# Kernel tuning notes

Hardware: AMD Instinct MI355X
Metric: run time of the kernel (lower is better)

## Reference

```python
import jax, jax.numpy as jnp
import numpy as np

V, H, L, S, B = 32000, 1024, 4, 256, 16


def setup_inputs() -> dict:
    key = jax.random.key(0)
    ks = jax.random.split(key, 6)
    s = 0.02  # init scale
    return {
        "x": jax.random.randint(ks[0], (S, B), 0, V, dtype=jnp.int32),
        "h0": jnp.zeros((L, B, H), jnp.float32),
        "c0": jnp.zeros((L, B, H), jnp.float32),
        "emb": jax.random.normal(ks[1], (V, H), jnp.float32) * s,
        "W_ih": jax.random.normal(ks[2], (L, 4 * H, H), jnp.float32) * s,
        "W_hh": jax.random.normal(ks[3], (L, 4 * H, H), jnp.float32) * s,
        "b_ih": jnp.zeros((L, 4 * H), jnp.float32),
        "b_hh": jnp.zeros((L, 4 * H), jnp.float32),
        "fc_W": jax.random.normal(ks[4], (V, H), jnp.float32) * s,
        "fc_b": jnp.zeros((V,), jnp.float32),
    }


def _lstm_layer(xs, h0, c0, Wih, Whh, b):
    # xs: [S, B, Hin]; torch gate order is (i, f, g, o)
    def step(carry, x_t):
        h, c = carry
        z = x_t @ Wih.T + h @ Whh.T + b  # [B, 4H]
        i, f, g, o = jnp.split(z, 4, axis=-1)
        c = jax.nn.sigmoid(f) * c + jax.nn.sigmoid(i) * jnp.tanh(g)
        h = jax.nn.sigmoid(o) * jnp.tanh(c)
        return (h, c), h

    (hT, cT), ys = jax.lax.scan(step, (h0, c0), xs)
    return ys, hT, cT


def reference(x, h0, c0, emb, W_ih, W_hh, b_ih, b_hh, fc_W, fc_b):
    y = emb[x]  # [S, B, H]
    h_fin, c_fin = [], []
    for l in range(L):  # fixed small layer count; time dim handled by scan
        y, hT, cT = _lstm_layer(y, h0[l], c0[l], W_ih[l], W_hh[l], b_ih[l] + b_hh[l])
        h_fin.append(hT)
        c_fin.append(cT)
    logits = y @ fc_W.T + fc_b  # [S, B, V]
    return logits, jnp.stack(h_fin), jnp.stack(c_fin)
```

## Files before the change

kernel.cpp:

```cpp
#include <hip/hip_runtime.h>
#include <hip/hip_bf16.h>

typedef unsigned short u16;
typedef short short8 __attribute__((ext_vector_type(8)));
typedef u16 u16x8 __attribute__((ext_vector_type(8)));
typedef float f32x4 __attribute__((ext_vector_type(4)));

#define H 1024
#define NB 16
#define SEQ 256
#define NL 4
#define VOCAB 32000
#define G4 4096
#define YSZ ((size_t)SEQ * NB * H)

__device__ __forceinline__ u16 f2bf(float f) {
  __hip_bfloat16 h = __float2bfloat16(f);
  return *reinterpret_cast<u16*>(&h);
}
__device__ __forceinline__ float sigm(float x) { return 1.0f / (1.0f + __expf(-x)); }
__device__ __forceinline__ float tanhfast(float x) { return 2.0f / (1.0f + __expf(-2.0f * x)) - 1.0f; }

__device__ __forceinline__ f32x4 mfma16(short8 a, short8 b, f32x4 c) {
  return __builtin_amdgcn_mfma_f32_16x16x32_bf16(a, b, c, 0, 0, 0);
}

template <int BOFF>
__device__ __forceinline__ short8 ldg_sc(const u16* p) {
  short8 r;
  asm volatile("global_load_dwordx4 %0, %1, off offset:%2 sc0 sc1"
               : "=&v"(r) : "v"(p), "n"(BOFF));
  return r;
}
template <int BOFF>
__device__ __forceinline__ short8 ldg_ca(const u16* p) {
  short8 r;
  asm volatile("global_load_dwordx4 %0, %1, off offset:%2"
               : "=&v"(r) : "v"(p), "n"(BOFF));
  return r;
}

#define LD8SC(d, p)                                            \
  do {                                                         \
    d[0] = ldg_sc<0 * 64>(p); d[1] = ldg_sc<1 * 64>(p);        \
    d[2] = ldg_sc<2 * 64>(p); d[3] = ldg_sc<3 * 64>(p);        \
    d[4] = ldg_sc<4 * 64>(p); d[5] = ldg_sc<5 * 64>(p);        \
    d[6] = ldg_sc<6 * 64>(p); d[7] = ldg_sc<7 * 64>(p);        \
  } while (0)
#define LD8CA(d, p)                                            \
  do {                                                         \
    d[0] = ldg_ca<0 * 64>(p); d[1] = ldg_ca<1 * 64>(p);        \
    d[2] = ldg_ca<2 * 64>(p); d[3] = ldg_ca<3 * 64>(p);        \
    d[4] = ldg_ca<4 * 64>(p); d[5] = ldg_ca<5 * 64>(p);        \
    d[6] = ldg_ca<6 * 64>(p); d[7] = ldg_ca<7 * 64>(p);        \
  } while (0)


__global__ void cvt_bf16(const float* __restrict__ in, u16* __restrict__ out, int n8) {
  const int i = blockIdx.x * blockDim.x + threadIdx.x;
  if (i >= n8) return;
  const float4 a = ((const float4*)in)[2 * i];
  const float4 b = ((const float4*)in)[2 * i + 1];
  u16x8 o;
  o[0] = f2bf(a.x); o[1] = f2bf(a.y); o[2] = f2bf(a.z); o[3] = f2bf(a.w);
  o[4] = f2bf(b.x); o[5] = f2bf(b.y); o[6] = f2bf(b.z); o[7] = f2bf(b.w);
  *(u16x8*)(out + (size_t)i * 8) = o;
}

__global__ void bias_sum(const float* __restrict__ a, const float* __restrict__ b,
                         float* __restrict__ o, int n) {
  const int i = blockIdx.x * blockDim.x + threadIdx.x;
  if (i < n) o[i] = a[i] + b[i];
}

__global__ void zero_u32(unsigned* __restrict__ p, int n) {
  const int i = blockIdx.x * blockDim.x + threadIdx.x;
  if (i < n) p[i] = 0u;
}

__global__ void gather_emb(const int* __restrict__ x, const float* __restrict__ emb,
                           u16* __restrict__ Y) {
  const int row = blockIdx.x;
  const int tok = x[row];
  const float4 v = ((const float4*)(emb + (size_t)tok * H))[threadIdx.x];
  ushort4 o;
  o.x = f2bf(v.x); o.y = f2bf(v.y); o.z = f2bf(v.z); o.w = f2bf(v.w);
  *(ushort4*)(Y + (size_t)row * H + threadIdx.x * 4) = o;
}

__device__ __forceinline__ void pollboth_sp(const unsigned* __restrict__ xp, unsigned xt,
                                            const unsigned* __restrict__ hp, unsigned ht) {
  unsigned xv, hv;
  do {
    asm volatile("global_load_dword %0, %2, off sc0 sc1\n\t"
                 "global_load_dword %1, %3, off sc0 sc1\n\t"
                 "s_waitcnt vmcnt(0)"
                 : "=&v"(xv), "=&v"(hv) : "v"(xp), "v"(hp) : "memory");
  } while (!__all(xv >= xt && hv >= ht));
  __builtin_amdgcn_sched_barrier(0);
}


__global__ __launch_bounds__(256, 1) void lstm_scan(
    const u16* __restrict__ ybase_r, u16* __restrict__ ybase_w,
    const u16* __restrict__ Wih_all, const u16* __restrict__ Whh_all,
    const float* __restrict__ bias_all, const u16* __restrict__ h0_all,
    const float* __restrict__ c0_all, float* __restrict__ hfin_all,
    float* __restrict__ cfin_all, unsigned* __restrict__ bars)
{
  extern __shared__ u16 sm[];
  u16* __restrict__ smw = sm;
  f32x4* __restrict__ lred = (f32x4*)(sm + 65536);
  u16* __restrict__ smh = sm + 73728;

  const int tid = threadIdx.x;
  const int lane = tid & 63;
  const int wid = tid >> 6;
  const int l = blockIdx.x >> 6;
  const int jgrp = blockIdx.x & 63;
  const int jbase = jgrp * 16;
  const int b = lane & 15;
  const int lg = lane >> 4;
  const int m = lane & 15;
  const int j = jbase + wid * 4 + lg;

  const u16* __restrict__ Yin  = ybase_r + (size_t)l * YSZ;
  u16* __restrict__ Yout       = ybase_w + (size_t)(l + 1) * YSZ;
  const u16* __restrict__ Wih  = Wih_all + (size_t)l * G4 * H;
  const u16* __restrict__ Whh  = Whh_all + (size_t)l * G4 * H;
  const float* __restrict__ bias = bias_all + (size_t)l * G4;
  const u16* __restrict__ h0b  = h0_all + (size_t)l * NB * H;
  const float* __restrict__ c0 = c0_all + (size_t)l * NB * H;
  float* __restrict__ hfin     = hfin_all + (size_t)l * NB * H;
  float* __restrict__ cfin     = cfin_all + (size_t)l * NB * H;
  unsigned* __restrict__ myflags = bars + l * 1024;
  const unsigned* __restrict__ xflags = bars + (l > 0 ? (l - 1) : 0) * 1024;
  unsigned* __restrict__ myflag_wr = myflags + jgrp * 16;
  const unsigned* __restrict__ xfp = xflags + lane * 16;
  const unsigned* __restrict__ hfp = myflags + lane * 16;

  #pragma unroll
  for (int rt = 0; rt < 4; ++rt) {
    const size_t ar = (size_t)((m & 3) * H + jbase + rt * 4 + (m >> 2));
    const u16* src = Whh + ar * H + lg * 8;
    #pragma unroll
    for (int i = 0; i < 8; ++i) {
      const int ks = wid * 8 + i;
      short8 w = *(const short8*)(src + ks * 32);
      *(short8*)(smw + (size_t)rt * 16384 + (size_t)ks * 512 + lane * 8) = w;
    }
  }
  short8 WI[32];
  #pragma unroll
  for (int rt = 0; rt < 4; ++rt) {
    const size_t ar = (size_t)((m & 3) * H + jbase + rt * 4 + (m >> 2));
    const u16* src = Wih + ar * H + lg * 8;
    #pragma unroll
    for (int i = 0; i < 8; ++i) {
      WI[rt * 8 + i] = *(const short8*)(src + (wid * 8 + i) * 32);
      asm volatile("" : "+v"(WI[rt * 8 + i]));
    }
  }
  __syncthreads();

  f32x4 bias4;
  bias4[0] = bias[0 * H + j];
  bias4[1] = bias[1 * H + j];
  bias4[2] = bias[2 * H + j];
  bias4[3] = bias[3 * H + j];

  float c = c0[b * H + j];
  const int boff = b * H + lg * 8;
  const int kboff = wid * 256;
  const u16* __restrict__ smwv = smw + (size_t)wid * 4096 + lane * 8;

  for (int t = 0; t < SEQ; ++t) {
    const u16* xw = Yin + (size_t)t * (NB * H) + boff + kboff;
    const u16* hw = (t == 0 ? h0b : Yout + (size_t)(t - 1) * (NB * H)) + boff + kboff;

    const unsigned xt = (l > 0) ? (unsigned)(t + 1) : 0u;
    const unsigned ht = (unsigned)t;
    if ((xt | ht) != 0u) pollboth_sp(xfp, xt, hfp, ht);

    short8 fx[8], fh[8];
    if (l > 0) { LD8SC(fx, xw); } else { LD8CA(fx, xw); }
    if (t > 0) { LD8SC(fh, hw); } else { LD8CA(fh, hw); }

    asm volatile("s_waitcnt vmcnt(8)" ::: "memory");
    __builtin_amdgcn_sched_barrier(0);

    f32x4 a0 = {0.f, 0.f, 0.f, 0.f};
    f32x4 a1 = {0.f, 0.f, 0.f, 0.f};
    f32x4 a2 = {0.f, 0.f, 0.f, 0.f};
    f32x4 a3 = {0.f, 0.f, 0.f, 0.f};

    #pragma unroll
    for (int i = 0; i < 8; ++i) {
      a0 = mfma16(WI[0 * 8 + i], fx[i], a0);
      a1 = mfma16(WI[1 * 8 + i], fx[i], a1);
      a2 = mfma16(WI[2 * 8 + i], fx[i], a2);
      a3 = mfma16(WI[3 * 8 + i], fx[i], a3);
    }

    __builtin_amdgcn_sched_barrier(0);
    asm volatile("s_waitcnt vmcnt(0)" ::: "memory");
    __builtin_amdgcn_sched_barrier(0);

    #pragma unroll
    for (int i = 0; i < 8; ++i) {
      short8 w0 = *(const short8*)(smwv + 0 * 16384 + i * 512);
      short8 w1 = *(const short8*)(smwv + 1 * 16384 + i * 512);
      short8 w2 = *(const short8*)(smwv + 2 * 16384 + i * 512);
      short8 w3 = *(const short8*)(smwv + 3 * 16384 + i * 512);
      a0 = mfma16(w0, fh[i], a0);
      a1 = mfma16(w1, fh[i], a1);
      a2 = mfma16(w2, fh[i], a2);
      a3 = mfma16(w3, fh[i], a3);
    }

    if (wid != 0) lred[(0 * 4 + wid) * 64 + lane] = a0;
    if (wid != 1) lred[(1 * 4 + wid) * 64 + lane] = a1;
    if (wid != 2) lred[(2 * 4 + wid) * 64 + lane] = a2;
    if (wid != 3) lred[(3 * 4 + wid) * 64 + lane] = a3;
    __syncthreads();

    f32x4 z4 = bias4;
    if (wid == 0)      z4 += a0;
    else if (wid == 1) z4 += a1;
    else if (wid == 2) z4 += a2;
    else               z4 += a3;
    #pragma unroll
    for (int w2 = 0; w2 < 4; ++w2)
      if (w2 != wid) z4 += lred[(wid * 4 + w2) * 64 + lane];

    const float ig = sigm(z4[0]);
    const float fg = sigm(z4[1]);
    const float gg = tanhfast(z4[2]);
    const float og = sigm(z4[3]);
    c = fg * c + ig * gg;
    const float h = og * tanhfast(c);

    smh[b * 16 + wid * 4 + lg] = f2bf(h);
    if (t == SEQ - 1) {
      hfin[b * H + j] = h;
      cfin[b * H + j] = c;
    }

    __syncthreads();
    if (wid == 0) {
      if (lane < 32) {
        const int br = lane >> 1, half = lane & 1;
        u16x8 pv = *(const u16x8*)&smh[br * 16 + half * 8];
        const u16* dst = Yout + (size_t)t * (NB * H) + (size_t)br * H + jbase + half * 8;
        asm volatile("global_store_dwordx4 %0, %1, off sc0 sc1"
                     :: "v"(dst), "v"(pv) : "memory");
      }
      asm volatile("s_waitcnt vmcnt(0)" ::: "memory");
      if (lane == 0) {
        const unsigned tv = (unsigned)(t + 1);
        asm volatile("global_store_dword %0, %1, off sc0 sc1"
                     :: "v"(myflag_wr), "v"(tv) : "memory");
      }
    }
  }
}


__global__ __launch_bounds__(256, 1) void gemm_bt_bias(
    const u16* __restrict__ A, const u16* __restrict__ Bw,
    const float* __restrict__ bias, float* __restrict__ C, int N)
{
  __shared__ u16 As[128 * 64];
  __shared__ u16 Bs[128 * 64];
  const int tid = threadIdx.x;
  const int lane = tid & 63;
  const int wid = tid >> 6;
  const unsigned id = blockIdx.x + gridDim.x * blockIdx.y;
  const unsigned xcd = id & 7u, seq = id >> 3;
  const int m0 = (int)(xcd * 4 + (seq & 3u)) * 128;
  const int n0 = (int)(seq >> 2) * 128;
  const int wr = wid >> 1, wc = wid & 1;
  const int lr = lane >> 3;
  const int lc = (lane & 7) * 8;
  f32x4 acc[4][4] = {};

  for (int k0 = 0; k0 < H; k0 += 64) {
    __syncthreads();
    #pragma unroll
    for (int cc = 0; cc < 4; ++cc) {
      const int row = wid * 32 + cc * 8 + lr;
      __builtin_amdgcn_global_load_lds(
          (const __attribute__((address_space(1))) void*)(A + (size_t)(m0 + row) * H + k0 + lc),
          (__attribute__((address_space(3))) void*)(As + row * 64 + lc), 16, 0, 0);
      __builtin_amdgcn_global_load_lds(
          (const __attribute__((address_space(1))) void*)(Bw + (size_t)(n0 + row) * H + k0 + lc),
          (__attribute__((address_space(3))) void*)(Bs + row * 64 + lc), 16, 0, 0);
    }
    __syncthreads();
    #pragma unroll
    for (int ks = 0; ks < 2; ++ks) {
      short8 af[4], bfr[4];
      #pragma unroll
      for (int i = 0; i < 4; ++i) {
        af[i]  = *(const short8*)&As[(wr * 64 + i * 16 + (lane & 15)) * 64 + ks * 32 + (lane >> 4) * 8];
        bfr[i] = *(const short8*)&Bs[(wc * 64 + i * 16 + (lane & 15)) * 64 + ks * 32 + (lane >> 4) * 8];
      }
      #pragma unroll
      for (int i = 0; i < 4; ++i) {
        #pragma unroll
        for (int jj = 0; jj < 4; ++jj)
          acc[i][jj] = mfma16(af[i], bfr[jj], acc[i][jj]);
      }
    }
  }

  #pragma unroll
  for (int jj = 0; jj < 4; ++jj) {
    const int col = n0 + wc * 64 + jj * 16 + (lane & 15);
    const float bv = bias[col];
    #pragma unroll
    for (int i = 0; i < 4; ++i) {
      const int rbase = m0 + wr * 64 + i * 16 + (lane >> 4) * 4;
      #pragma unroll
      for (int r = 0; r < 4; ++r)
        C[(size_t)(rbase + r) * N + col] = acc[i][jj][r] + bv;
    }
  }
}


extern "C" void kernel_launch(void* const* d_in, const int* in_sizes, int n_in,
                              void* d_out, int out_size, void* d_ws, size_t ws_size,
                              hipStream_t stream) {
  const int*   x    = (const int*)d_in[0];
  const float* h0   = (const float*)d_in[1];
  const float* c0   = (const float*)d_in[2];
  const float* emb  = (const float*)d_in[3];
  const float* W_ih = (const float*)d_in[4];
  const float* W_hh = (const float*)d_in[5];
  const float* b_ih = (const float*)d_in[6];
  const float* b_hh = (const float*)d_in[7];
  const float* fc_W = (const float*)d_in[8];
  const float* fc_b = (const float*)d_in[9];
  float* out = (float*)d_out;
  char* ws = (char*)d_ws;

  size_t off = 0;
  u16* WihB = (u16*)(ws + off); off += (size_t)NL * G4 * H * 2;
  u16* WhhB = (u16*)(ws + off); off += (size_t)NL * G4 * H * 2;
  u16* fcWB = (u16*)(ws + off); off += (size_t)VOCAB * H * 2;
  u16* h0B  = (u16*)(ws + off); off += (size_t)NL * NB * H * 2;
  float* biasB = (float*)(ws + off); off += (size_t)NL * G4 * 4;
  u16* ybufs = (u16*)(ws + off); off += (size_t)(NL + 1) * YSZ * 2;
  unsigned* bars = (unsigned*)(ws + off); off += 16384;
  if (ws_size < off) return;

  int n8;
  n8 = NL * G4 * H / 8;  cvt_bf16<<<(n8 + 255) / 256, 256, 0, stream>>>(W_ih, WihB, n8);
  n8 = NL * G4 * H / 8;  cvt_bf16<<<(n8 + 255) / 256, 256, 0, stream>>>(W_hh, WhhB, n8);
  n8 = VOCAB * H / 8;    cvt_bf16<<<(n8 + 255) / 256, 256, 0, stream>>>(fc_W, fcWB, n8);
  n8 = NL * NB * H / 8;  cvt_bf16<<<(n8 + 255) / 256, 256, 0, stream>>>(h0, h0B, n8);
  bias_sum<<<(NL * G4 + 255) / 256, 256, 0, stream>>>(b_ih, b_hh, biasB, NL * G4);
  zero_u32<<<16, 256, 0, stream>>>(bars, 4096);
  gather_emb<<<SEQ * NB, 256, 0, stream>>>(x, emb, ybufs);

  float* hfin = out + (size_t)SEQ * NB * VOCAB;
  float* cfin = hfin + (size_t)NL * NB * H;

  lstm_scan<<<NL * 64, 256, 147968, stream>>>(
      ybufs, ybufs, WihB, WhhB, biasB, h0B, c0, hfin, cfin, bars);

  gemm_bt_bias<<<dim3(32, 250), 256, 0, stream>>>(
      ybufs + (size_t)NL * YSZ, fcWB, fc_b, out, VOCAB);
}
```

Before: 1.955 ms.

## Replace flag-based cross-block sync with sentinel-filled data polling

Drops the separate per-block step flags. The output Y buffers for layers 1-4 are now pre-filled with an all-ones sentinel, and consumers spin-load the actual h/x data until no 32-bit word equals the sentinel. This removes the flag store, its vmcnt(0) drain on the producer side and the flag-then-data round trip on the consumer side, so each step avoids a dependent global access. The risks are the extra fill kernel over 4 layers of Y, heavier polling traffic because full data tiles are re-read on every retry, and correctness depending on bf16 pairs never naturally encoding as 0xFFFFFFFF (a NaN pattern) and on the 16-byte stores landing atomically.

```diff
diff --git a/kernel.cpp b/kernel.cpp
--- a/kernel.cpp
+++ b/kernel.cpp
@@ -5,6 +5,7 @@
 typedef short short8 __attribute__((ext_vector_type(8)));
 typedef u16 u16x8 __attribute__((ext_vector_type(8)));
 typedef float f32x4 __attribute__((ext_vector_type(4)));
+typedef unsigned u32x4v __attribute__((ext_vector_type(4)));
 
 #define H 1024
 #define NB 16
@@ -13,6 +14,7 @@
 #define VOCAB 32000
 #define G4 4096
 #define YSZ ((size_t)SEQ * NB * H)
+#define SENT 0xFFFFFFFFu
 
 __device__ __forceinline__ u16 f2bf(float f) {
   __hip_bfloat16 h = __float2bfloat16(f);
@@ -55,6 +57,19 @@
     d[6] = ldg_ca<6 * 64>(p); d[7] = ldg_ca<7 * 64>(p);        \
   } while (0)
 
+__device__ __forceinline__ unsigned maxpk(const short8 (&f)[8]) {
+  unsigned mx = 0u;
+  #pragma unroll
+  for (int i = 0; i < 8; ++i) {
+    u32x4v d = __builtin_bit_cast(u32x4v, f[i]);
+    mx = d[0] > mx ? d[0] : mx;
+    mx = d[1] > mx ? d[1] : mx;
+    mx = d[2] > mx ? d[2] : mx;
+    mx = d[3] > mx ? d[3] : mx;
+  }
+  return mx;
+}
+
 
 __global__ void cvt_bf16(const float* __restrict__ in, u16* __restrict__ out, int n8) {
   const int i = blockIdx.x * blockDim.x + threadIdx.x;
@@ -73,9 +88,10 @@
   if (i < n) o[i] = a[i] + b[i];
 }
 
-__global__ void zero_u32(unsigned* __restrict__ p, int n) {
+__global__ void fill_sent(u32x4v* __restrict__ p) {
   const int i = blockIdx.x * blockDim.x + threadIdx.x;
-  if (i < n) p[i] = 0u;
+  u32x4v v = {SENT, SENT, SENT, SENT};
+  p[i] = v;
 }
 
 __global__ void gather_emb(const int* __restrict__ x, const float* __restrict__ emb,
@@ -88,25 +104,13 @@
   *(ushort4*)(Y + (size_t)row * H + threadIdx.x * 4) = o;
 }
 
-__device__ __forceinline__ void pollboth_sp(const unsigned* __restrict__ xp, unsigned xt,
-                                            const unsigned* __restrict__ hp, unsigned ht) {
-  unsigned xv, hv;
-  do {
-    asm volatile("global_load_dword %0, %2, off sc0 sc1\n\t"
-                 "global_load_dword %1, %3, off sc0 sc1\n\t"
-                 "s_waitcnt vmcnt(0)"
-                 : "=&v"(xv), "=&v"(hv) : "v"(xp), "v"(hp) : "memory");
-  } while (!__all(xv >= xt && hv >= ht));
-  __builtin_amdgcn_sched_barrier(0);
-}
-
 
 __global__ __launch_bounds__(256, 1) void lstm_scan(
     const u16* __restrict__ ybase_r, u16* __restrict__ ybase_w,
     const u16* __restrict__ Wih_all, const u16* __restrict__ Whh_all,
     const float* __restrict__ bias_all, const u16* __restrict__ h0_all,
     const float* __restrict__ c0_all, float* __restrict__ hfin_all,
-    float* __restrict__ cfin_all, unsigned* __restrict__ bars)
+    float* __restrict__ cfin_all)
 {
   extern __shared__ u16 sm[];
   u16* __restrict__ smw = sm;
@@ -133,11 +137,6 @@
   const float* __restrict__ c0 = c0_all + (size_t)l * NB * H;
   float* __restrict__ hfin     = hfin_all + (size_t)l * NB * H;
   float* __restrict__ cfin     = cfin_all + (size_t)l * NB * H;
-  unsigned* __restrict__ myflags = bars + l * 1024;
-  const unsigned* __restrict__ xflags = bars + (l > 0 ? (l - 1) : 0) * 1024;
-  unsigned* __restrict__ myflag_wr = myflags + jgrp * 16;
-  const unsigned* __restrict__ xfp = xflags + lane * 16;
-  const unsigned* __restrict__ hfp = myflags + lane * 16;
 
   #pragma unroll
   for (int rt = 0; rt < 4; ++rt) {
@@ -178,16 +177,28 @@
     const u16* xw = Yin + (size_t)t * (NB * H) + boff + kboff;
     const u16* hw = (t == 0 ? h0b : Yout + (size_t)(t - 1) * (NB * H)) + boff + kboff;
 
-    const unsigned xt = (l > 0) ? (unsigned)(t + 1) : 0u;
-    const unsigned ht = (unsigned)t;
-    if ((xt | ht) != 0u) pollboth_sp(xfp, xt, hfp, ht);
-
     short8 fx[8], fh[8];
-    if (l > 0) { LD8SC(fx, xw); } else { LD8CA(fx, xw); }
-    if (t > 0) { LD8SC(fh, hw); } else { LD8CA(fh, hw); }
-
-    asm volatile("s_waitcnt vmcnt(8)" ::: "memory");
-    __builtin_amdgcn_sched_barrier(0);
+    const bool needx = (l > 0);
+    const bool needh = (t > 0);
+    if (!needx) LD8CA(fx, xw);
+    if (!needh) LD8CA(fh, hw);
+
+    if (needx || needh) {
+      unsigned ok;
+      do {
+        if (needx) LD8SC(fx, xw);
+        if (needh) LD8SC(fh, hw);
+        asm volatile("s_waitcnt vmcnt(0)" ::: "memory");
+        unsigned mx = 0u;
+        if (needx) { unsigned a = maxpk(fx); mx = a > mx ? a : mx; }
+        if (needh) { unsigned a = maxpk(fh); mx = a > mx ? a : mx; }
+        ok = (mx != SENT);
+      } while (!__all(ok));
+      __builtin_amdgcn_sched_barrier(0);
+    } else {
+      asm volatile("s_waitcnt vmcnt(0)" ::: "memory");
+      __builtin_amdgcn_sched_barrier(0);
+    }
 
     f32x4 a0 = {0.f, 0.f, 0.f, 0.f};
     f32x4 a1 = {0.f, 0.f, 0.f, 0.f};
@@ -201,11 +212,6 @@
       a2 = mfma16(WI[2 * 8 + i], fx[i], a2);
       a3 = mfma16(WI[3 * 8 + i], fx[i], a3);
     }
-
-    __builtin_amdgcn_sched_barrier(0);
-    asm volatile("s_waitcnt vmcnt(0)" ::: "memory");
-    __builtin_amdgcn_sched_barrier(0);
-
     #pragma unroll
     for (int i = 0; i < 8; ++i) {
       short8 w0 = *(const short8*)(smwv + 0 * 16384 + i * 512);
@@ -247,20 +253,12 @@
     }
 
     __syncthreads();
-    if (wid == 0) {
-      if (lane < 32) {
-        const int br = lane >> 1, half = lane & 1;
-        u16x8 pv = *(const u16x8*)&smh[br * 16 + half * 8];
-        const u16* dst = Yout + (size_t)t * (NB * H) + (size_t)br * H + jbase + half * 8;
-        asm volatile("global_store_dwordx4 %0, %1, off sc0 sc1"
-                     :: "v"(dst), "v"(pv) : "memory");
-      }
-      asm volatile("s_waitcnt vmcnt(0)" ::: "memory");
-      if (lane == 0) {
-        const unsigned tv = (unsigned)(t + 1);
-        asm volatile("global_store_dword %0, %1, off sc0 sc1"
-                     :: "v"(myflag_wr), "v"(tv) : "memory");
-      }
+    if (wid == 0 && lane < 32) {
+      const int br = lane >> 1, half = lane & 1;
+      u16x8 pv = *(const u16x8*)&smh[br * 16 + half * 8];
+      const u16* dst = Yout + (size_t)t * (NB * H) + (size_t)br * H + jbase + half * 8;
+      asm volatile("global_store_dwordx4 %0, %1, off sc0 sc1"
+                   :: "v"(dst), "v"(pv) : "memory");
     }
   }
 }
@@ -352,7 +350,6 @@
   u16* h0B  = (u16*)(ws + off); off += (size_t)NL * NB * H * 2;
   float* biasB = (float*)(ws + off); off += (size_t)NL * G4 * 4;
   u16* ybufs = (u16*)(ws + off); off += (size_t)(NL + 1) * YSZ * 2;
-  unsigned* bars = (unsigned*)(ws + off); off += 16384;
   if (ws_size < off) return;
 
   int n8;
@@ -361,14 +358,14 @@
   n8 = VOCAB * H / 8;    cvt_bf16<<<(n8 + 255) / 256, 256, 0, stream>>>(fc_W, fcWB, n8);
   n8 = NL * NB * H / 8;  cvt_bf16<<<(n8 + 255) / 256, 256, 0, stream>>>(h0, h0B, n8);
   bias_sum<<<(NL * G4 + 255) / 256, 256, 0, stream>>>(b_ih, b_hh, biasB, NL * G4);
-  zero_u32<<<16, 256, 0, stream>>>(bars, 4096);
+  fill_sent<<<8192, 256, 0, stream>>>((u32x4v*)(ybufs + YSZ));
   gather_emb<<<SEQ * NB, 256, 0, stream>>>(x, emb, ybufs);
 
   float* hfin = out + (size_t)SEQ * NB * VOCAB;
   float* cfin = hfin + (size_t)NL * NB * H;
 
   lstm_scan<<<NL * 64, 256, 147968, stream>>>(
-      ybufs, ybufs, WihB, WhhB, biasB, h0B, c0, hfin, cfin, bars);
+      ybufs, ybufs, WihB, WhhB, biasB, h0B, c0, hfin, cfin);
 
   gemm_bt_bias<<<dim3(32, 250), 256, 0, stream>>>(
       ybufs + (size_t)NL * YSZ, fcWB, fc_b, out, VOCAB);
```

New measurement: 1.664 ms. -14.9%, faster.
